# Optimization experiments

Measured on AMD Instinct MI355X. Metric: run time of the kernel, lower is better.

Reference implementation:

```python
import jax, jax.numpy as jnp
import numpy as np

SCORE_THRESH = 0.25
NMS_THRESH = 0.45
DETECTIONS = 100   # self.detections
K_CAND = 300       # fixed pre-NMS candidate count (jit-friendly stand-in for torch.where filtering)
STRIDES = (8, 16, 32)


def setup_inputs() -> dict:
    key = jax.random.key(0)
    ks = jax.random.split(key, 5)
    pred_p3 = jax.random.normal(ks[0], (16, 80, 80, 3, 85), jnp.float32)
    pred_p4 = jax.random.normal(ks[1], (16, 40, 40, 3, 85), jnp.float32)
    pred_p5 = jax.random.normal(ks[2], (16, 20, 20, 3, 85), jnp.float32)
    anchors = jnp.array([[[10, 13], [16, 30], [33, 23]],
                         [[30, 61], [62, 45], [59, 119]],
                         [[116, 90], [156, 198], [373, 326]]], jnp.float32)
    image_shapes = jnp.full((16, 2), 640, jnp.int32)  # (h, w) per image
    scale_factors = jax.random.uniform(ks[3], (16,), jnp.float32, 0.5, 1.5)
    return {"pred_p3": pred_p3, "pred_p4": pred_p4, "pred_p5": pred_p5,
            "anchors": anchors, "image_shapes": image_shapes,
            "scale_factors": scale_factors, "max_size": 4096}


def _decode_level(p, stride, anchor_wh):
    # p: [B,H,W,A,5+C] already sigmoided
    B, H, W, A, _ = p.shape
    gx = jnp.arange(W, dtype=p.dtype)
    gy = jnp.arange(H, dtype=p.dtype)
    grid = jnp.stack(jnp.meshgrid(gx, gy, indexing='xy'), axis=-1)  # [H,W,2] = (x,y)
    xy = (2.0 * p[..., :2] - 0.5 + grid[None, :, :, None, :]) * stride
    wh = 4.0 * p[..., 2:4] ** 2 * anchor_wh  # anchor_wh: [A,2]
    box = jnp.concatenate([xy, wh], axis=-1).reshape(B, H * W * A, 4)
    obj = p[..., 4].reshape(B, H * W * A)
    cls = p[..., 5:].reshape(B, H * W * A, -1)
    return box, obj, cls


def _pairwise_iou(b):  # b: [K,4] xyxy
    area = (b[:, 2] - b[:, 0]) * (b[:, 3] - b[:, 1])
    lt = jnp.maximum(b[:, None, :2], b[None, :, :2])
    rb = jnp.minimum(b[:, None, 2:], b[None, :, 2:])
    wh = jnp.clip(rb - lt, 0.0)
    inter = wh[..., 0] * wh[..., 1]
    return inter / (area[:, None] + area[None, :] - inter + 1e-9)


def _nms_image(boxes, scores, labels, im_shape, scale, max_size):
    # boxes [K,4], scores [K] sorted desc, labels [K] int
    w = im_shape[1].astype(boxes.dtype)
    h = im_shape[0].astype(boxes.dtype)
    boxes = jnp.stack([jnp.clip(boxes[:, 0], 0.0, w), jnp.clip(boxes[:, 1], 0.0, h),
                       jnp.clip(boxes[:, 2], 0.0, w), jnp.clip(boxes[:, 3], 0.0, h)], axis=1)
    # class-offset boxes (batched_nms)
    bn = jax.lax.stop_gradient(boxes + (labels.astype(boxes.dtype) * max_size)[:, None])
    iou = _pairwise_iou(bn)
    s_ng = jax.lax.stop_gradient(scores)
    K = boxes.shape[0]
    ar = jnp.arange(K)

    def body(i, keep):
        active = keep[i] & (s_ng[i] > SCORE_THRESH)
        return keep & ~((iou[i] > NMS_THRESH) & (ar > i) & active)

    keep = jax.lax.fori_loop(0, K, body, jnp.ones(K, bool))
    final = jnp.where(keep & (s_ng > SCORE_THRESH), scores, 0.0)
    det_s, det_i = jax.lax.top_k(final, DETECTIONS)
    det_b = boxes[det_i] / scale
    det_l = labels[det_i].astype(boxes.dtype)
    return jnp.concatenate([det_b, det_s[:, None], det_l[:, None]], axis=1)  # [D,6]


def reference(pred_p3, pred_p4, pred_p5, anchors, image_shapes, scale_factors, max_size):
    boxes_l, obj_l, cls_l = [], [], []
    for i, (pred, stride) in enumerate(zip((pred_p3, pred_p4, pred_p5), STRIDES)):
        p = jax.nn.sigmoid(pred)
        b, o, c = _decode_level(p, float(stride), anchors[i])
        boxes_l.append(b); obj_l.append(o); cls_l.append(c)
    boxes = jnp.concatenate(boxes_l, axis=1)   # [B,N,4] cxcywh
    obj = jnp.concatenate(obj_l, axis=1)       # [B,N]
    cls = jnp.concatenate(cls_l, axis=1)       # [B,N,C]
    # cxcywh -> xyxy
    cx, cy, ww, hh = boxes[..., 0], boxes[..., 1], boxes[..., 2], boxes[..., 3]
    boxes = jnp.stack([cx - ww / 2, cy - hh / 2, cx + ww / 2, cy + hh / 2], axis=-1)
    B, N, C = cls.shape
    logits = obj[..., None] * cls              # [B,N,C]
    valid = (obj[..., None] > SCORE_THRESH) & (logits > SCORE_THRESH)
    flat = jnp.where(valid, logits, 0.0).reshape(B, N * C)
    vals, idx = jax.lax.top_k(flat, K_CAND)    # sorted desc per image
    aidx = idx // C
    labels = idx % C
    cand_boxes = jnp.take_along_axis(boxes, aidx[..., None], axis=1)  # [B,K,4]
    out = jax.vmap(_nms_image, in_axes=(0, 0, 0, 0, 0, None))(
        cand_boxes, vals, labels, image_shapes, scale_factors, jnp.float32(max_size))
    return out  # [B, DETECTIONS, 6] = (x1,y1,x2,y2,score,label)
```

## Files before the change

### kernel.cpp

```cpp
#include <hip/hip_runtime.h>
#include <cstdint>
#include <cstddef>

#define BATCH 16
#define NCLS 80
#define NANCH 25200
#define G 48
#define NCHUNK 525
#define CPB 7
#define NBMAX 75
#define ABINS 512
#define SBINS 1024
#define SCAP 2048
#define SCAP2 4096
#define LCAP 1024
#define KC 300
#define DET 100
#define SCORE_T 0.25f
#define NMS_T 0.45f
#define NBLK 50
#define SPAN 504
#define CNTPAD 16

__device__ __forceinline__ float sg(float x) { return 1.0f / (1.0f + expf(-x)); }

__device__ __forceinline__ const float* anchor_base(const float* p3, const float* p4,
                                                    const float* p5, int b, int n) {
    if (n < 19200) return p3 + ((size_t)b * 19200 + n) * 85;
    if (n < 24000) return p4 + ((size_t)b * 4800 + (n - 19200)) * 85;
    return p5 + ((size_t)b * 1200 + (n - 24000)) * 85;
}

struct Chunk { const float4* p; int outbase; int b; };
__device__ __forceinline__ Chunk chunk_of(int g, const float* p3, const float* p4,
                                          const float* p5) {
    Chunk ck;
    int b = g / NCHUNK, ch = g % NCHUNK;
    const float* src; int a0, lvlN, gbase;
    if (ch < 400)      { src = p3; a0 = ch * G;         lvlN = 19200; gbase = 0; }
    else if (ch < 500) { src = p4; a0 = (ch - 400) * G; lvlN = 4800;  gbase = 19200; }
    else               { src = p5; a0 = (ch - 500) * G; lvlN = 1200;  gbase = 24000; }
    ck.p = (const float4*)(src + ((size_t)b * lvlN + a0) * 85);
    ck.outbase = b * NANCH + gbase + a0;
    ck.b = b;
    return ck;
}

__global__ __launch_bounds__(256) void k_max(const float* __restrict__ p3,
                                             const float* __restrict__ p4,
                                             const float* __restrict__ p5,
                                             float* __restrict__ gmax,
                                             unsigned int* __restrict__ ahist) {
    __shared__ __align__(16) float buf[2][G * 85];
    __shared__ float pmax[5 * G];
    int tid = threadIdx.x;
    int b = blockIdx.x / NBMAX;
    int j = blockIdx.x % NBMAX;
    int g0 = b * NCHUNK + j * CPB;

    float4 pre[4];
    Chunk c0 = chunk_of(g0, p3, p4, p5);
#pragma unroll
    for (int r = 0; r < 4; r++) {
        int i = tid + r * 256;
        pre[r] = (i < (G * 85 / 4)) ? c0.p[i] : make_float4(0.f, 0.f, 0.f, 0.f);
    }
#pragma unroll
    for (int r = 0; r < 4; r++) {
        int i = tid + r * 256;
        if (i < (G * 85 / 4)) ((float4*)buf[0])[i] = pre[r];
    }
    {
        Chunk c1 = chunk_of(g0 + 1, p3, p4, p5);
#pragma unroll
        for (int r = 0; r < 4; r++) {
            int i = tid + r * 256;
            pre[r] = (i < (G * 85 / 4)) ? c1.p[i] : make_float4(0.f, 0.f, 0.f, 0.f);
        }
    }
    __syncthreads();

    for (int t = 0; t < CPB; ++t) {
        const float* cur = buf[t & 1];
        if (tid < 240) {
            int a = tid % G, part = tid / G;
            const float* base = cur + a * 85 + 5 + part * 16;
            float m = base[0];
#pragma unroll
            for (int k = 1; k < 16; k++) m = fmaxf(m, base[k]);
            pmax[part * G + a] = m;
        }
        __syncthreads();
        if (tid < G) {
            Chunk me = chunk_of(g0 + t, p3, p4, p5);
            float m = pmax[tid];
#pragma unroll
            for (int p = 1; p < 5; p++) m = fmaxf(m, pmax[p * G + tid]);
            float obj = sg(cur[tid * 85 + 4]);
            float v = 0.0f;
            if (obj > SCORE_T) v = obj * sg(m);
            gmax[me.outbase + tid] = v;
            if (v > SCORE_T) {
                int bin = (int)((v - SCORE_T) * (ABINS / 0.75f));
                bin = bin < 0 ? 0 : (bin > ABINS - 1 ? ABINS - 1 : bin);
                atomicAdd(&ahist[b * ABINS + bin], 1u);
            }
        }
        if (t + 1 < CPB) {
#pragma unroll
            for (int r = 0; r < 4; r++) {
                int i = tid + r * 256;
                if (i < (G * 85 / 4)) ((float4*)buf[(t + 1) & 1])[i] = pre[r];
            }
            if (t + 2 < CPB) {
                Chunk cn = chunk_of(g0 + t + 2, p3, p4, p5);
#pragma unroll
                for (int r = 0; r < 4; r++) {
                    int i = tid + r * 256;
                    pre[r] = (i < (G * 85 / 4)) ? cn.p[i] : make_float4(0.f, 0.f, 0.f, 0.f);
                }
            }
        }
        __syncthreads();
    }
}

__global__ __launch_bounds__(512) void k_collect(
    const float* __restrict__ p3, const float* __restrict__ p4, const float* __restrict__ p5,
    const float* __restrict__ gmax, const unsigned int* __restrict__ ahist,
    unsigned int* __restrict__ shist, unsigned int* __restrict__ scnt,
    float* __restrict__ ss, unsigned int* __restrict__ sidx) {
    __shared__ unsigned int h[ABINS];
    __shared__ unsigned int wtot[8], wsuf[8];
    __shared__ int TaS;
    __shared__ int an[SPAN];
    __shared__ float og[SPAN];
    __shared__ float lss[LCAP];
    __shared__ unsigned int lsi[LCAP];
    __shared__ unsigned int ncand, lcnt, gbase;
    int tid = threadIdx.x;
    int lane = tid & 63, wv = tid >> 6;
    int b = blockIdx.x / NBLK;
    int blk = blockIdx.x % NBLK;
    if (tid == 0) { ncand = 0u; TaS = 0; lcnt = 0u; }

    unsigned int run = ahist[b * ABINS + tid];
#pragma unroll
    for (int off = 1; off < 64; off <<= 1) {
        unsigned int v = __shfl_down(run, off, 64);
        if (lane + off < 64) run += v;
    }
    if (lane == 0) wtot[wv] = run;
    __syncthreads();
    if (wv == 0) {
        unsigned int r = (lane < 8) ? wtot[lane] : 0u;
#pragma unroll
        for (int off = 1; off < 8; off <<= 1) {
            unsigned int v = __shfl_down(r, off, 64);
            if (lane + off < 8) r += v;
        }
        if (lane < 8) wsuf[lane] = r;
    }
    __syncthreads();
    unsigned int suf = run + ((wv < 7) ? wsuf[wv + 1] : 0u);
    h[tid] = suf;
    __syncthreads();
    if (suf >= KC && (tid == ABINS - 1 || h[tid + 1] < KC)) TaS = tid;
    __syncthreads();
    int Ta = TaS;

    int n0 = blk * SPAN;
    for (int i = tid; i < SPAN; i += 512) {
        int n = n0 + i;
        float v = gmax[(size_t)b * NANCH + n];
        if (v > SCORE_T) {
            int bin = (int)((v - SCORE_T) * (ABINS / 0.75f));
            bin = bin < 0 ? 0 : (bin > ABINS - 1 ? ABINS - 1 : bin);
            if (bin >= Ta) {
                unsigned int p = atomicAdd(&ncand, 1u);
                an[p] = n;
            }
        }
    }
    __syncthreads();
    int M = (int)ncand;
    for (int i = tid; i < M; i += 512) {
        const float* pb = anchor_base(p3, p4, p5, b, an[i]);
        og[i] = sg(pb[4]);
    }
    __syncthreads();
    int twoTa = 2 * Ta;
    for (int idx = tid; idx < M * NCLS; idx += 512) {
        int a = idx / NCLS, c = idx - a * NCLS;
        const float* pb = anchor_base(p3, p4, p5, b, an[a]);
        float s = og[a] * sg(pb[5 + c]);
        if (s > SCORE_T) {
            int bin = (int)((s - SCORE_T) * (SBINS / 0.75f));
            bin = bin < 0 ? 0 : (bin > SBINS - 1 ? SBINS - 1 : bin);
            if (bin >= twoTa) {
                atomicAdd(&shist[b * SBINS + bin], 1u);
                unsigned int p = atomicAdd(&lcnt, 1u);
                if (p < LCAP) {
                    lss[p] = s;
                    lsi[p] = (unsigned int)(an[a] * NCLS + c);
                } else {
                    unsigned int q = atomicAdd(&scnt[b * CNTPAD], 1u);
                    if (q < SCAP2) {
                        ss[(size_t)b * SCAP2 + q] = s;
                        sidx[(size_t)b * SCAP2 + q] = (unsigned int)(an[a] * NCLS + c);
                    }
                }
            }
        }
    }
    __syncthreads();
    unsigned int nl = lcnt < LCAP ? lcnt : LCAP;
    if (tid == 0 && nl > 0) gbase = atomicAdd(&scnt[b * CNTPAD], nl);
    __syncthreads();
    for (unsigned int i = tid; i < nl; i += 512) {
        unsigned int p = gbase + i;
        if (p < SCAP2) {
            ss[(size_t)b * SCAP2 + p] = lss[i];
            sidx[(size_t)b * SCAP2 + p] = lsi[i];
        }
    }
}

struct NmsBuf {
    unsigned long long msk[KC * 5];
    float4 bx[KC];
    int lab[KC];
    float sc2[KC];
    float ar[KC];
    unsigned long long keep[5];
    unsigned int actw[10];
    int wpref[6];
    int order[DET];
    int okept[DET];
};

__global__ __launch_bounds__(1024) void k_img(
    const float* __restrict__ p3, const float* __restrict__ p4, const float* __restrict__ p5,
    const float* __restrict__ anchors, const int* __restrict__ imshapes,
    const float* __restrict__ scalef,
    const unsigned int* __restrict__ shist, const unsigned int* __restrict__ scnt_g,
    const float* __restrict__ ss, const unsigned int* __restrict__ sidx,
    float* __restrict__ out) {
    __shared__ unsigned int hist[SBINS];
    __shared__ __align__(16) NmsBuf u;
    __shared__ float cs[SCAP];
    __shared__ unsigned int ci[SCAP];
    __shared__ float sv[KC];
    __shared__ unsigned int si[KC];
    __shared__ unsigned int wtot[16], wsuf[16];
    __shared__ unsigned int scnt_s;
    __shared__ int TsS;

    int b = blockIdx.x;
    int tid = threadIdx.x;
    int lane = tid & 63, wv = tid >> 6;
    if (tid == 0) { scnt_s = 0u; TsS = 0; }

    unsigned int run = shist[b * SBINS + tid];
#pragma unroll
    for (int off = 1; off < 64; off <<= 1) {
        unsigned int v = __shfl_down(run, off, 64);
        if (lane + off < 64) run += v;
    }
    if (lane == 0) wtot[wv] = run;
    __syncthreads();
    if (wv == 0) {
        unsigned int r = (lane < 16) ? wtot[lane] : 0u;
#pragma unroll
        for (int off = 1; off < 16; off <<= 1) {
            unsigned int v = __shfl_down(r, off, 64);
            if (lane + off < 16) r += v;
        }
        if (lane < 16) wsuf[lane] = r;
    }
    __syncthreads();
    unsigned int suf = run + ((wv < 15) ? wsuf[wv + 1] : 0u);
    hist[tid] = suf;
    __syncthreads();
    if (suf >= KC && (tid == SBINS - 1 || hist[tid + 1] < KC)) TsS = tid;
    __syncthreads();
    int Ts = TsS;

    unsigned int total = scnt_g[b * CNTPAD];
    int navail = (int)(total < SCAP2 ? total : SCAP2);
    for (int i = tid; i < navail; i += 1024) {
        float s = ss[(size_t)b * SCAP2 + i];
        int bin = (int)((s - SCORE_T) * (SBINS / 0.75f));
        bin = bin < 0 ? 0 : (bin > SBINS - 1 ? SBINS - 1 : bin);
        if (bin >= Ts) {
            unsigned int pos = atomicAdd(&scnt_s, 1u);
            if (pos < SCAP) { cs[pos] = s; ci[pos] = sidx[(size_t)b * SCAP2 + i]; }
        }
    }
    __syncthreads();
    int nc = (int)(scnt_s < SCAP ? scnt_s : SCAP);

    if (tid < KC) { sv[tid] = 0.f; si[tid] = 0xffffffffu; }
    __syncthreads();
    for (int i = tid; i < nc; i += 1024) {
        float s = cs[i];
        unsigned int ii = ci[i];
        int r = 0;
        for (int j = 0; j < nc; j++) {
            float sj = cs[j];
            unsigned int ij = ci[j];
            if (sj > s || (sj == s && ij < ii)) r++;
        }
        if (r < KC) { sv[r] = s; si[r] = ii; }
    }
    __syncthreads();
    int valid = nc < KC ? nc : KC;

    if (tid < KC) {
        int i = tid;
        if (i < valid) {
            unsigned int fi = si[i];
            int n = (int)(fi / NCLS), c = (int)(fi % NCLS);
            int lvl = (n < 19200) ? 0 : (n < 24000 ? 1 : 2);
            const int offl[3] = {0, 19200, 24000};
            const int Wl[3] = {80, 40, 20};
            const int cntl[3] = {19200, 4800, 1200};
            const float strl[3] = {8.f, 16.f, 32.f};
            const float* pp = lvl == 0 ? p3 : (lvl == 1 ? p4 : p5);
            int nl = n - offl[lvl];
            int a = nl % 3, cell = nl / 3;
            int gx = cell % Wl[lvl], gy = cell / Wl[lvl];
            const float* pb = pp + ((size_t)b * cntl[lvl] + nl) * 85;
            float s0 = sg(pb[0]), s1 = sg(pb[1]), s2 = sg(pb[2]), s3 = sg(pb[3]);
            float stride = strl[lvl];
            float aw = anchors[(lvl * 3 + a) * 2 + 0];
            float ah = anchors[(lvl * 3 + a) * 2 + 1];
            float cx = (2.0f * s0 - 0.5f + (float)gx) * stride;
            float cy = (2.0f * s1 - 0.5f + (float)gy) * stride;
            float bw = 4.0f * s2 * s2 * aw;
            float bh = 4.0f * s3 * s3 * ah;
            float hf = (float)imshapes[b * 2 + 0];
            float wf = (float)imshapes[b * 2 + 1];
            float x1 = cx - bw / 2.0f, y1 = cy - bh / 2.0f;
            float x2 = cx + bw / 2.0f, y2 = cy + bh / 2.0f;
            x1 = fminf(fmaxf(x1, 0.f), wf);
            y1 = fminf(fmaxf(y1, 0.f), hf);
            x2 = fminf(fmaxf(x2, 0.f), wf);
            y2 = fminf(fmaxf(y2, 0.f), hf);
            u.bx[i] = make_float4(x1, y1, x2, y2);
            u.lab[i] = c;
            u.sc2[i] = sv[i];
            u.ar[i] = (x2 - x1) * (y2 - y1);
        } else {
            u.bx[i] = make_float4(0, 0, 0, 0);
            u.lab[i] = -1 - i;
            u.sc2[i] = 0.f;
            u.ar[i] = 0.f;
        }
    }
    __syncthreads();

    if (tid < 10) u.actw[tid] = 0u;
    for (int t = tid; t < KC * 5; t += 1024) {
        int i = t / 5, w = t % 5;
        float4 bi = u.bx[i];
        int li = u.lab[i];
        float ai = u.ar[i];
        unsigned long long m = 0ull;
        for (int tb = 0; tb < 64; tb++) {
            int j = w * 64 + tb;
            if (j < KC && j > i && u.lab[j] == li) {
                float4 bj = u.bx[j];
                float ltx = fmaxf(bi.x, bj.x), lty = fmaxf(bi.y, bj.y);
                float rbx = fminf(bi.z, bj.z), rby = fminf(bi.w, bj.w);
                float iw = fmaxf(rbx - ltx, 0.f), ih = fmaxf(rby - lty, 0.f);
                float inter = iw * ih;
                float iou = inter / (ai + u.ar[j] - inter + 1e-9f);
                if (iou > NMS_T) m |= (1ull << tb);
            }
        }
        u.msk[t] = m;
    }
    __syncthreads();

    for (int i = tid; i < KC; i += 1024) {
        unsigned long long nz = u.msk[i * 5] | u.msk[i * 5 + 1] | u.msk[i * 5 + 2] |
                                u.msk[i * 5 + 3] | u.msk[i * 5 + 4];
        if (nz) atomicOr(&u.actw[i >> 5], 1u << (i & 31));
    }
    __syncthreads();
    if (tid == 0) {
        u.keep[0] = u.keep[1] = u.keep[2] = u.keep[3] = u.keep[4] = ~0ull;
        for (int w = 0; w < 10; w++) {
            unsigned int mw = u.actw[w];
            while (mw) {
                int bpos = __ffs(mw) - 1;
                mw &= mw - 1;
                int i = w * 32 + bpos;
                if ((u.keep[i >> 6] >> (i & 63)) & 1ull) {
#pragma unroll
                    for (int r = 0; r < 5; r++) u.keep[r] &= ~u.msk[i * 5 + r];
                }
            }
        }
        int s = 0;
        for (int w = 0; w < 5; w++) {
            unsigned long long kw = u.keep[w];
            if (w == 4) kw &= (1ull << 44) - 1ull;
            u.wpref[w] = s;
            s += (int)__popcll(kw);
        }
        u.wpref[5] = s;
    }
    __syncthreads();

    if (tid < KC) {
        int w = tid >> 6, bp = tid & 63;
        unsigned long long kw = u.keep[w];
        bool kept = (kw >> bp) & 1ull;
        int r = u.wpref[w] + (int)__popcll(kw & ((1ull << bp) - 1ull));
        if (kept) {
            if (r < DET) { u.order[r] = tid; u.okept[r] = 1; }
        } else {
            int nr = u.wpref[5] + (tid - r);
            if (nr < DET) { u.order[nr] = tid; u.okept[nr] = 0; }
        }
    }
    __syncthreads();

    if (tid < DET) {
        int o = u.order[tid];
        float scale = scalef[b];
        float4 bb = u.bx[o];
        float s = (u.okept[tid] && o < valid) ? u.sc2[o] : 0.f;
        float lb = (o < valid) ? (float)u.lab[o] : 0.f;
        float* po = out + ((size_t)b * DET + tid) * 6;
        po[0] = bb.x / scale;
        po[1] = bb.y / scale;
        po[2] = bb.z / scale;
        po[3] = bb.w / scale;
        po[4] = s;
        po[5] = lb;
    }
}

extern "C" void kernel_launch(void* const* d_in, const int* in_sizes, int n_in,
                              void* d_out, int out_size, void* d_ws, size_t ws_size,
                              hipStream_t stream) {
    const float* p3 = (const float*)d_in[0];
    const float* p4 = (const float*)d_in[1];
    const float* p5 = (const float*)d_in[2];
    const float* anchors = (const float*)d_in[3];
    const int* imshapes = (const int*)d_in[4];
    const float* scalef = (const float*)d_in[5];
    float* out = (float*)d_out;

    char* ws = (char*)d_ws;
    float* gmax = (float*)ws;
    unsigned int* ahist = (unsigned int*)(ws + 1612800);
    unsigned int* shist = (unsigned int*)(ws + 1612800 + 32768);
    unsigned int* scnt  = (unsigned int*)(ws + 1612800 + 32768 + 65536);
    float* ss           = (float*)(ws + 1612800 + 32768 + 65536 + 1024);
    unsigned int* sidx  = (unsigned int*)(ws + 1612800 + 32768 + 65536 + 1024 + 262144);

    hipMemsetAsync(ws + 1612800, 0, 32768 + 65536 + 1024, stream);

    k_max<<<BATCH * NBMAX, 256, 0, stream>>>(p3, p4, p5, gmax, ahist);
    k_collect<<<BATCH * NBLK, 512, 0, stream>>>(p3, p4, p5, gmax, ahist, shist, scnt, ss, sidx);
    k_img<<<BATCH, 1024, 0, stream>>>(p3, p4, p5, anchors, imshapes, scalef,
                                      shist, scnt, ss, sidx, out);
}
```

Before: 230.0 us.

## Restructure k_max into per-wave 16-anchor tiles with shuffle reductions and no block barriers

Replaces the block-level double-buffered chunk pipeline in k_max with independent per-wavefront tiles of 16 anchors. Each wave loads its tile into a private LDS slot, and four lanes per anchor compute the class max, combined with xor shuffles. This removes __syncthreads and the software prefetch, relying on many resident waves to hide memory latency, and launches 1575 blocks in a grid-stride loop. The risk is lower per-wave load depth and the loss of explicit prefetch overlap. There is also no explicit wave barrier between the LDS writes and the reads that other lanes make, which relies on in-wave execution ordering.

```diff
diff --git a/kernel.cpp b/kernel.cpp
--- a/kernel.cpp
+++ b/kernel.cpp
@@ -5,10 +5,6 @@
 #define BATCH 16
 #define NCLS 80
 #define NANCH 25200
-#define G 48
-#define NCHUNK 525
-#define CPB 7
-#define NBMAX 75
 #define ABINS 512
 #define SBINS 1024
 #define SCAP 2048
@@ -22,6 +18,10 @@
 #define SPAN 504
 #define CNTPAD 16
 
+#define TILES_PER_IMG 1575
+#define TOT_TILES (BATCH * TILES_PER_IMG)
+#define KMAX_BLOCKS 1575
+
 __device__ __forceinline__ float sg(float x) { return 1.0f / (1.0f + expf(-x)); }
 
 __device__ __forceinline__ const float* anchor_base(const float* p3, const float* p4,
@@ -31,97 +31,60 @@
     return p5 + ((size_t)b * 1200 + (n - 24000)) * 85;
 }
 
-struct Chunk { const float4* p; int outbase; int b; };
-__device__ __forceinline__ Chunk chunk_of(int g, const float* p3, const float* p4,
-                                          const float* p5) {
-    Chunk ck;
-    int b = g / NCHUNK, ch = g % NCHUNK;
-    const float* src; int a0, lvlN, gbase;
-    if (ch < 400)      { src = p3; a0 = ch * G;         lvlN = 19200; gbase = 0; }
-    else if (ch < 500) { src = p4; a0 = (ch - 400) * G; lvlN = 4800;  gbase = 19200; }
-    else               { src = p5; a0 = (ch - 500) * G; lvlN = 1200;  gbase = 24000; }
-    ck.p = (const float4*)(src + ((size_t)b * lvlN + a0) * 85);
-    ck.outbase = b * NANCH + gbase + a0;
-    ck.b = b;
-    return ck;
-}
-
 __global__ __launch_bounds__(256) void k_max(const float* __restrict__ p3,
                                              const float* __restrict__ p4,
                                              const float* __restrict__ p5,
                                              float* __restrict__ gmax,
                                              unsigned int* __restrict__ ahist) {
-    __shared__ __align__(16) float buf[2][G * 85];
-    __shared__ float pmax[5 * G];
+    __shared__ __align__(16) float4 wbuf[4][340];
     int tid = threadIdx.x;
-    int b = blockIdx.x / NBMAX;
-    int j = blockIdx.x % NBMAX;
-    int g0 = b * NCHUNK + j * CPB;
-
-    float4 pre[4];
-    Chunk c0 = chunk_of(g0, p3, p4, p5);
-#pragma unroll
-    for (int r = 0; r < 4; r++) {
-        int i = tid + r * 256;
-        pre[r] = (i < (G * 85 / 4)) ? c0.p[i] : make_float4(0.f, 0.f, 0.f, 0.f);
-    }
-#pragma unroll
-    for (int r = 0; r < 4; r++) {
-        int i = tid + r * 256;
-        if (i < (G * 85 / 4)) ((float4*)buf[0])[i] = pre[r];
-    }
-    {
-        Chunk c1 = chunk_of(g0 + 1, p3, p4, p5);
-#pragma unroll
-        for (int r = 0; r < 4; r++) {
-            int i = tid + r * 256;
-            pre[r] = (i < (G * 85 / 4)) ? c1.p[i] : make_float4(0.f, 0.f, 0.f, 0.f);
-        }
-    }
-    __syncthreads();
-
-    for (int t = 0; t < CPB; ++t) {
-        const float* cur = buf[t & 1];
-        if (tid < 240) {
-            int a = tid % G, part = tid / G;
-            const float* base = cur + a * 85 + 5 + part * 16;
-            float m = base[0];
-#pragma unroll
-            for (int k = 1; k < 16; k++) m = fmaxf(m, base[k]);
-            pmax[part * G + a] = m;
-        }
-        __syncthreads();
-        if (tid < G) {
-            Chunk me = chunk_of(g0 + t, p3, p4, p5);
-            float m = pmax[tid];
-#pragma unroll
-            for (int p = 1; p < 5; p++) m = fmaxf(m, pmax[p * G + tid]);
-            float obj = sg(cur[tid * 85 + 4]);
+    int lane = tid & 63, wv = tid >> 6;
+    float4* slot = wbuf[wv];
+    const float* sf = (const float*)slot;
+    int wid = blockIdx.x * 4 + wv;
+    int g = lane >> 2, r = lane & 3;
+
+    for (int t = wid; t < TOT_TILES; t += KMAX_BLOCKS * 4) {
+        int b = t / TILES_PER_IMG, lt = t % TILES_PER_IMG;
+        const float* src; int gidx;
+        if (lt < 1200)      { src = p3 + ((size_t)b * 19200 + lt * 16) * 85;          gidx = lt * 16; }
+        else if (lt < 1500) { src = p4 + ((size_t)b * 4800 + (lt - 1200) * 16) * 85;  gidx = 19200 + (lt - 1200) * 16; }
+        else                { src = p5 + ((size_t)b * 1200 + (lt - 1500) * 16) * 85;  gidx = 24000 + (lt - 1500) * 16; }
+        const float4* tp = (const float4*)src;
+
+        float4 v0 = tp[lane];
+        float4 v1 = tp[lane + 64];
+        float4 v2 = tp[lane + 128];
+        float4 v3 = tp[lane + 192];
+        float4 v4 = tp[lane + 256];
+        float4 v5 = make_float4(0.f, 0.f, 0.f, 0.f);
+        bool ex = lane < 20;
+        if (ex) v5 = tp[lane + 320];
+        slot[lane] = v0;
+        slot[lane + 64] = v1;
+        slot[lane + 128] = v2;
+        slot[lane + 192] = v3;
+        slot[lane + 256] = v4;
+        if (ex) slot[lane + 320] = v5;
+
+        const float* cb = sf + 85 * g + 5 + 20 * r;
+        float m = cb[0];
+#pragma unroll
+        for (int k = 1; k < 20; k++) m = fmaxf(m, cb[k]);
+        m = fmaxf(m, __shfl_xor(m, 1, 64));
+        m = fmaxf(m, __shfl_xor(m, 2, 64));
+
+        if (r == 0) {
+            float obj = sg(sf[85 * g + 4]);
             float v = 0.0f;
             if (obj > SCORE_T) v = obj * sg(m);
-            gmax[me.outbase + tid] = v;
+            gmax[(size_t)b * NANCH + gidx + g] = v;
             if (v > SCORE_T) {
                 int bin = (int)((v - SCORE_T) * (ABINS / 0.75f));
                 bin = bin < 0 ? 0 : (bin > ABINS - 1 ? ABINS - 1 : bin);
                 atomicAdd(&ahist[b * ABINS + bin], 1u);
             }
         }
-        if (t + 1 < CPB) {
-#pragma unroll
-            for (int r = 0; r < 4; r++) {
-                int i = tid + r * 256;
-                if (i < (G * 85 / 4)) ((float4*)buf[(t + 1) & 1])[i] = pre[r];
-            }
-            if (t + 2 < CPB) {
-                Chunk cn = chunk_of(g0 + t + 2, p3, p4, p5);
-#pragma unroll
-                for (int r = 0; r < 4; r++) {
-                    int i = tid + r * 256;
-                    pre[r] = (i < (G * 85 / 4)) ? cn.p[i] : make_float4(0.f, 0.f, 0.f, 0.f);
-                }
-            }
-        }
-        __syncthreads();
     }
 }
 
@@ -465,7 +428,7 @@
 
     hipMemsetAsync(ws + 1612800, 0, 32768 + 65536 + 1024, stream);
 
-    k_max<<<BATCH * NBMAX, 256, 0, stream>>>(p3, p4, p5, gmax, ahist);
+    k_max<<<KMAX_BLOCKS, 256, 0, stream>>>(p3, p4, p5, gmax, ahist);
     k_collect<<<BATCH * NBLK, 512, 0, stream>>>(p3, p4, p5, gmax, ahist, shist, scnt, ss, sidx);
     k_img<<<BATCH, 1024, 0, stream>>>(p3, p4, p5, anchors, imshapes, scalef,
                                       shist, scnt, ss, sidx, out);
```

New measurement: 234.7 us. 1.02x slower.
